# Kernel optimization log

Measured on AMD Instinct MI355X. Metric: run time of the kernel, lower is better.

The kernel has to match this reference:

```python
import jax, jax.numpy as jnp
import numpy as np

B = 512
INPUT_DIM = 1536
MAMBA_DIM = 1024
OUTPUT_DIM = 1024
D_STATE = 128
D_CONV = 4
EXPAND = 2
HEADDIM = 64
D_INNER = EXPAND * MAMBA_DIM          # 2048, == d_ssm
NHEADS = D_INNER // HEADDIM           # 32
CONV_DIM = D_INNER + 2 * D_STATE      # 2304
D_IN_PROJ = 2 * D_INNER + 2 * D_STATE + NHEADS  # 4384 (d_mlp = 0)
EPS = 1e-5


def rms_norm(x, g):
    return x * jax.lax.rsqrt(jnp.mean(x * x, axis=-1, keepdims=True) + EPS) * g


def setup_inputs() -> dict:
    key = jax.random.key(0)
    ks = jax.random.split(key, 16)
    def lin(k, fan_in, shape):
        return jax.random.normal(k, shape, jnp.float32) / np.sqrt(fan_in)
    return {
        "x": jax.random.normal(ks[0], (B, INPUT_DIM), jnp.float32),
        "conv_state": jax.random.normal(ks[1], (B, CONV_DIM, D_CONV), jnp.float32),
        "ssm_state": jax.random.normal(ks[2], (B, NHEADS, HEADDIM, D_STATE), jnp.float32),
        # NormedLinear in_proj (Linear + RMSNorm + SiLU)
        "w_in": lin(ks[3], INPUT_DIM, (INPUT_DIM, MAMBA_DIM)),
        "b_in": jnp.zeros((MAMBA_DIM,), jnp.float32),
        "g_in": jnp.ones((MAMBA_DIM,), jnp.float32),
        # Mamba2 params
        "W_inproj": lin(ks[4], MAMBA_DIM, (MAMBA_DIM, D_IN_PROJ)),
        "conv_w": lin(ks[5], D_CONV, (CONV_DIM, D_CONV)),
        "conv_b": jnp.zeros((CONV_DIM,), jnp.float32),
        "A_log": jnp.log(jax.random.uniform(ks[6], (NHEADS,), jnp.float32, 1.0, 16.0)),
        "dt_bias": 0.1 * jax.random.normal(ks[7], (NHEADS,), jnp.float32),
        "D": jnp.ones((NHEADS,), jnp.float32),
        "W_mamba_out": lin(ks[8], D_INNER, (D_INNER, MAMBA_DIM)),
        # outer out_proj Linear + RMSNorm
        "w_out": lin(ks[9], MAMBA_DIM, (MAMBA_DIM, OUTPUT_DIM)),
        "b_out": jnp.zeros((OUTPUT_DIM,), jnp.float32),
        "g_outnorm": jnp.ones((OUTPUT_DIM,), jnp.float32),
    }


def reference(x, conv_state, ssm_state, w_in, b_in, g_in, W_inproj, conv_w, conv_b,
              A_log, dt_bias, D, W_mamba_out, w_out, b_out, g_outnorm):
    # in_proj: Linear -> RMSNorm -> SiLU
    h = jax.nn.silu(rms_norm(x @ w_in + b_in, g_in))          # [B, MAMBA_DIM]
    zxbcdt = h @ W_inproj                                      # [B, D_IN_PROJ]
    z = zxbcdt[:, :D_INNER]                                    # [B, D_INNER]
    xbc = zxbcdt[:, D_INNER:D_INNER + CONV_DIM]                # [B, CONV_DIM]
    dt = zxbcdt[:, D_INNER + CONV_DIM:]                        # [B, NHEADS]
    # conv shift-and-sum
    conv_state_new = jnp.concatenate([conv_state[:, :, 1:], xbc[:, :, None]], axis=-1)
    xbc = jnp.sum(conv_state_new * conv_w[None], axis=-1) + conv_b
    xbc = jax.nn.silu(xbc)
    xh = xbc[:, :D_INNER].reshape(B, NHEADS, HEADDIM)          # [B, H, P]
    b = xbc[:, D_INNER:D_INNER + D_STATE]                      # [B, N]
    c = xbc[:, D_INNER + D_STATE:]                             # [B, N]
    # SSM step
    a = -jnp.exp(A_log)                                        # [H]
    dt = jax.nn.softplus(dt + dt_bias)                         # [B, H]
    da = jnp.exp(dt * a)                                       # [B, H]
    dbx = jnp.einsum('bh,bn,bhp->bhpn', dt, b, xh)
    ssm_state_new = ssm_state * da[:, :, None, None] + dbx     # [B, H, P, N]
    y = jnp.einsum('bhpn,bn->bhp', ssm_state_new, c)
    y = y + D[None, :, None] * xh
    y = y.reshape(B, D_INNER) * jax.nn.silu(z)
    y = y @ W_mamba_out                                        # [B, MAMBA_DIM]
    # outer projection + norm
    y = rms_norm(y @ w_out + b_out, g_outnorm)                 # [B, OUTPUT_DIM]
    return y, conv_state_new, ssm_state_new
```

## Files before the change

### kernel.cpp

```cpp
#include <hip/hip_runtime.h>
#include <hip/hip_bf16.h>

#define B_SZ      512
#define INPUT_DIM 1536
#define MAMBA_DIM 1024
#define OUT_DIM   1024
#define D_STATE   128
#define HEADDIM   64
#define D_INNER   2048
#define NHEADS    32
#define CONV_DIM  2304
#define D_IN_PROJ 4384

__device__ __forceinline__ float silu_precise(float x) {
    return x / (1.0f + expf(-x));
}

__global__ __launch_bounds__(256) void sgemm_kernel(
    const float* __restrict__ A, const float* __restrict__ W,
    const float* __restrict__ bias, float* __restrict__ C,
    int M, int N, int K)
{
    __shared__ float As[32][64];
    __shared__ float Bs[32][64];

    const int t   = threadIdx.x;
    const int bn0 = blockIdx.x * 64;
    const int bm0 = blockIdx.y * 64;
    const int tr  = t >> 4;
    const int tc  = t & 15;

    float acc[4][4] = {};

    for (int k0 = 0; k0 < K; k0 += 32) {
        #pragma unroll
        for (int i = 0; i < 2; ++i) {
            int idx = t + i * 256;
            int row = idx >> 3;
            int c4  = (idx & 7) * 4;
            float4 v = *(const float4*)(A + (size_t)(bm0 + row) * K + k0 + c4);
            As[c4 + 0][row] = v.x;
            As[c4 + 1][row] = v.y;
            As[c4 + 2][row] = v.z;
            As[c4 + 3][row] = v.w;
        }
        #pragma unroll
        for (int i = 0; i < 2; ++i) {
            int idx = t + i * 256;
            int kr  = idx >> 4;
            int c4  = (idx & 15) * 4;
            int n   = bn0 + c4;
            float4 v = make_float4(0.f, 0.f, 0.f, 0.f);
            if (n < N) v = *(const float4*)(W + (size_t)(k0 + kr) * N + n);
            *(float4*)&Bs[kr][c4] = v;
        }
        __syncthreads();

        #pragma unroll
        for (int k = 0; k < 32; ++k) {
            float4 a = *(const float4*)&As[k][tr * 4];
            float4 b = *(const float4*)&Bs[k][tc * 4];
            float av[4] = {a.x, a.y, a.z, a.w};
            float bv[4] = {b.x, b.y, b.z, b.w};
            #pragma unroll
            for (int i = 0; i < 4; ++i)
                #pragma unroll
                for (int j = 0; j < 4; ++j)
                    acc[i][j] += av[i] * bv[j];
        }
        __syncthreads();
    }

    #pragma unroll
    for (int i = 0; i < 4; ++i) {
        int m = bm0 + tr * 4 + i;
        #pragma unroll
        for (int j = 0; j < 4; ++j) {
            int n = bn0 + tc * 4 + j;
            if (n < N) {
                float v = acc[i][j];
                if (bias) v += bias[n];
                C[(size_t)m * N + n] = v;
            }
        }
    }
}

template <bool SILU>
__global__ __launch_bounds__(256) void rmsnorm_kernel(
    const float* __restrict__ X, const float* __restrict__ g,
    float* __restrict__ Y)
{
    const int row = blockIdx.x;
    const float* x = X + (size_t)row * 1024;
    float4 v = *(const float4*)(x + threadIdx.x * 4);
    float ss = v.x * v.x + v.y * v.y + v.z * v.z + v.w * v.w;
    #pragma unroll
    for (int off = 32; off > 0; off >>= 1) ss += __shfl_down(ss, off);

    __shared__ float wsum[4];
    const int wid = threadIdx.x >> 6;
    if ((threadIdx.x & 63) == 0) wsum[wid] = ss;
    __syncthreads();
    const float tot = wsum[0] + wsum[1] + wsum[2] + wsum[3];
    const float rs = 1.0f / sqrtf(tot * (1.0f / 1024.0f) + 1e-5f);

    float4 gv = *(const float4*)(g + threadIdx.x * 4);
    float4 o;
    o.x = v.x * rs * gv.x;
    o.y = v.y * rs * gv.y;
    o.z = v.z * rs * gv.z;
    o.w = v.w * rs * gv.w;
    if (SILU) {
        o.x = silu_precise(o.x);
        o.y = silu_precise(o.y);
        o.z = silu_precise(o.z);
        o.w = silu_precise(o.w);
    }
    *(float4*)(Y + (size_t)row * 1024 + threadIdx.x * 4) = o;
}

__global__ __launch_bounds__(256) void conv_kernel(
    const float* __restrict__ conv_state, const float* __restrict__ zx,
    const float* __restrict__ conv_w, const float* __restrict__ conv_b,
    float* __restrict__ conv_state_out, float* __restrict__ xbc_out)
{
    const int gid = blockIdx.x * 256 + threadIdx.x;
    const int b = gid / CONV_DIM;
    const int c = gid - b * CONV_DIM;

    float4 cs = *(const float4*)(conv_state + (size_t)gid * 4);
    float xn = zx[(size_t)b * D_IN_PROJ + D_INNER + c];
    float4 w = *(const float4*)(conv_w + c * 4);

    float s = cs.y * w.x + cs.z * w.y + cs.w * w.z + xn * w.w + conv_b[c];
    float r = silu_precise(s);

    float4 o = make_float4(cs.y, cs.z, cs.w, xn);
    *(float4*)(conv_state_out + (size_t)gid * 4) = o;
    xbc_out[gid] = r;
}

__global__ __launch_bounds__(256) void ssm_kernel(
    const float* __restrict__ ssm_state, const float* __restrict__ xbc,
    const float* __restrict__ zx, const float* __restrict__ A_log,
    const float* __restrict__ dt_bias, const float* __restrict__ Dp,
    float* __restrict__ ssm_out, float* __restrict__ yz)
{
    const int h = blockIdx.x;
    const int b = blockIdx.y;
    const int t = threadIdx.x;
    const int lane_n = t & 31;
    const int n0 = lane_n * 4;
    const int pg = t >> 5;

    float dtv = zx[(size_t)b * D_IN_PROJ + (D_INNER + CONV_DIM) + h] + dt_bias[h];
    dtv = (dtv > 20.f) ? dtv : log1pf(expf(dtv));
    const float a  = -expf(A_log[h]);
    const float da = expf(dtv * a);
    const float dcoef = Dp[h];

    const float* xrow = xbc + (size_t)b * CONV_DIM;

    const float4 bb = *(const float4*)(xrow + D_INNER + n0);
    const float4 cc = *(const float4*)(xrow + D_INNER + D_STATE + n0);

    const size_t slab = ((size_t)b * NHEADS + h) * (HEADDIM * D_STATE);
    const float* sp = ssm_state + slab;
    float*       so = ssm_out   + slab;

    #pragma unroll
    for (int i = 0; i < 8; ++i) {
        const int p = pg + i * 8;
        const float xh = xrow[h * HEADDIM + p];
        const float coef = dtv * xh;

        const size_t off = (size_t)p * D_STATE + n0;
        float4 s = *(const float4*)(sp + off);
        float4 ns;
        ns.x = s.x * da + coef * bb.x;
        ns.y = s.y * da + coef * bb.y;
        ns.z = s.z * da + coef * bb.z;
        ns.w = s.w * da + coef * bb.w;
        *(float4*)(so + off) = ns;

        float y = ns.x * cc.x + ns.y * cc.y + ns.z * cc.z + ns.w * cc.w;
        y += __shfl_xor(y, 16);
        y += __shfl_xor(y, 8);
        y += __shfl_xor(y, 4);
        y += __shfl_xor(y, 2);
        y += __shfl_xor(y, 1);

        if (lane_n == 0) {
            float z = zx[(size_t)b * D_IN_PROJ + h * HEADDIM + p];
            float yv = y + dcoef * xh;
            yz[(size_t)b * D_INNER + h * HEADDIM + p] = yv * silu_precise(z);
        }
    }
}


extern "C" void kernel_launch(void* const* d_in, const int* in_sizes, int n_in,
                              void* d_out, int out_size, void* d_ws, size_t ws_size,
                              hipStream_t stream)
{
    const float* x          = (const float*)d_in[0];
    const float* conv_state = (const float*)d_in[1];
    const float* ssm_state  = (const float*)d_in[2];
    const float* w_in       = (const float*)d_in[3];
    const float* b_in       = (const float*)d_in[4];
    const float* g_in       = (const float*)d_in[5];
    const float* W_inproj   = (const float*)d_in[6];
    const float* conv_w     = (const float*)d_in[7];
    const float* conv_b     = (const float*)d_in[8];
    const float* A_log      = (const float*)d_in[9];
    const float* dt_bias    = (const float*)d_in[10];
    const float* Dp         = (const float*)d_in[11];
    const float* W_mamba_out= (const float*)d_in[12];
    const float* w_out      = (const float*)d_in[13];
    const float* b_out      = (const float*)d_in[14];
    const float* g_outnorm  = (const float*)d_in[15];

    float* out_y    = (float*)d_out;
    float* out_conv = out_y + (size_t)B_SZ * OUT_DIM;
    float* out_ssm  = out_conv + (size_t)B_SZ * CONV_DIM * 4;

    float* ws  = (float*)d_ws;
    float* t1  = ws;
    float* h   = t1  + (size_t)B_SZ * MAMBA_DIM;
    float* zx  = h   + (size_t)B_SZ * MAMBA_DIM;
    float* xbc = zx  + (size_t)B_SZ * D_IN_PROJ;
    float* yzb = xbc + (size_t)B_SZ * CONV_DIM;
    float* u   = yzb + (size_t)B_SZ * D_INNER;
    float* t2  = u   + (size_t)B_SZ * MAMBA_DIM;

    sgemm_kernel<<<dim3(MAMBA_DIM / 64, B_SZ / 64), 256, 0, stream>>>(
        x, w_in, b_in, t1, B_SZ, MAMBA_DIM, INPUT_DIM);
    rmsnorm_kernel<true><<<B_SZ, 256, 0, stream>>>(t1, g_in, h);
    sgemm_kernel<<<dim3((D_IN_PROJ + 63) / 64, B_SZ / 64), 256, 0, stream>>>(
        h, W_inproj, nullptr, zx, B_SZ, D_IN_PROJ, MAMBA_DIM);
    conv_kernel<<<(B_SZ * CONV_DIM) / 256, 256, 0, stream>>>(
        conv_state, zx, conv_w, conv_b, out_conv, xbc);
    ssm_kernel<<<dim3(NHEADS, B_SZ), 256, 0, stream>>>(
        ssm_state, xbc, zx, A_log, dt_bias, Dp, out_ssm, yzb);
    sgemm_kernel<<<dim3(MAMBA_DIM / 64, B_SZ / 64), 256, 0, stream>>>(
        yzb, W_mamba_out, nullptr, u, B_SZ, MAMBA_DIM, D_INNER);
    sgemm_kernel<<<dim3(OUT_DIM / 64, B_SZ / 64), 256, 0, stream>>>(
        u, w_out, b_out, t2, B_SZ, OUT_DIM, MAMBA_DIM);
    rmsnorm_kernel<false><<<B_SZ, 256, 0, stream>>>(t2, g_outnorm, out_y);
}
```

Baseline: 1.321 ms.

## Split-K all GEMMs with atomic accumulation into zeroed workspace

Every GEMM now splits the K dimension across a third grid axis (8 or 4 slices), and partial tiles are accumulated into the output with float atomicAdd. A zero kernel clears the contiguous GEMM output buffers first. The workspace is reordered so those buffers sit together, and the A shared tile is padded to cut bank conflicts. The aim is more blocks to fill the GPU's many compute units, since the original grids were only 128–552 blocks. In exchange it adds atomic traffic, an extra zeroing pass, and non-deterministic summation order.

New measurement: 1.273 ms. 1.04x faster.

```diff
diff --git a/kernel.cpp b/kernel.cpp
--- a/kernel.cpp
+++ b/kernel.cpp
@@ -16,23 +16,33 @@
     return x / (1.0f + expf(-x));
 }
 
-__global__ __launch_bounds__(256) void sgemm_kernel(
+__global__ __launch_bounds__(256) void zero_kernel(float4* __restrict__ p, int n4)
+{
+    int i = blockIdx.x * 256 + threadIdx.x;
+    const int stride = gridDim.x * 256;
+    const float4 z = make_float4(0.f, 0.f, 0.f, 0.f);
+    for (; i < n4; i += stride) p[i] = z;
+}
+
+__global__ __launch_bounds__(256) void sgemm_splitk_kernel(
     const float* __restrict__ A, const float* __restrict__ W,
     const float* __restrict__ bias, float* __restrict__ C,
-    int M, int N, int K)
-{
-    __shared__ float As[32][64];
+    int M, int N, int K, int Kper)
+{
+    __shared__ float As[32][68];
     __shared__ float Bs[32][64];
 
     const int t   = threadIdx.x;
     const int bn0 = blockIdx.x * 64;
     const int bm0 = blockIdx.y * 64;
+    const int kz0 = blockIdx.z * Kper;
     const int tr  = t >> 4;
     const int tc  = t & 15;
 
     float acc[4][4] = {};
 
-    for (int k0 = 0; k0 < K; k0 += 32) {
+    for (int kk = 0; kk < Kper; kk += 32) {
+        const int k0 = kz0 + kk;
         #pragma unroll
         for (int i = 0; i < 2; ++i) {
             int idx = t + i * 256;
@@ -71,6 +81,7 @@
         __syncthreads();
     }
 
+    const bool addb = (bias != nullptr) && (blockIdx.z == 0);
     #pragma unroll
     for (int i = 0; i < 4; ++i) {
         int m = bm0 + tr * 4 + i;
@@ -79,8 +90,8 @@
             int n = bn0 + tc * 4 + j;
             if (n < N) {
                 float v = acc[i][j];
-                if (bias) v += bias[n];
-                C[(size_t)m * N + n] = v;
+                if (addb) v += bias[n];
+                atomicAdd(&C[(size_t)m * N + n], v);
             }
         }
     }
@@ -227,25 +238,29 @@
 
     float* ws  = (float*)d_ws;
     float* t1  = ws;
-    float* h   = t1  + (size_t)B_SZ * MAMBA_DIM;
-    float* zx  = h   + (size_t)B_SZ * MAMBA_DIM;
-    float* xbc = zx  + (size_t)B_SZ * D_IN_PROJ;
+    float* zx  = t1  + (size_t)B_SZ * MAMBA_DIM;
+    float* u   = zx  + (size_t)B_SZ * D_IN_PROJ;
+    float* t2  = u   + (size_t)B_SZ * MAMBA_DIM;
+    float* h   = t2  + (size_t)B_SZ * MAMBA_DIM;
+    float* xbc = h   + (size_t)B_SZ * MAMBA_DIM;
     float* yzb = xbc + (size_t)B_SZ * CONV_DIM;
-    float* u   = yzb + (size_t)B_SZ * D_INNER;
-    float* t2  = u   + (size_t)B_SZ * MAMBA_DIM;
-
-    sgemm_kernel<<<dim3(MAMBA_DIM / 64, B_SZ / 64), 256, 0, stream>>>(
-        x, w_in, b_in, t1, B_SZ, MAMBA_DIM, INPUT_DIM);
+
+    const int gemm_out_floats = B_SZ * (MAMBA_DIM + D_IN_PROJ + MAMBA_DIM + MAMBA_DIM);
+
+    zero_kernel<<<2048, 256, 0, stream>>>((float4*)ws, gemm_out_floats / 4);
+
+    sgemm_splitk_kernel<<<dim3(MAMBA_DIM / 64, B_SZ / 64, 8), 256, 0, stream>>>(
+        x, w_in, b_in, t1, B_SZ, MAMBA_DIM, INPUT_DIM, INPUT_DIM / 8);
     rmsnorm_kernel<true><<<B_SZ, 256, 0, stream>>>(t1, g_in, h);
-    sgemm_kernel<<<dim3((D_IN_PROJ + 63) / 64, B_SZ / 64), 256, 0, stream>>>(
-        h, W_inproj, nullptr, zx, B_SZ, D_IN_PROJ, MAMBA_DIM);
+    sgemm_splitk_kernel<<<dim3((D_IN_PROJ + 63) / 64, B_SZ / 64, 4), 256, 0, stream>>>(
+        h, W_inproj, nullptr, zx, B_SZ, D_IN_PROJ, MAMBA_DIM, MAMBA_DIM / 4);
     conv_kernel<<<(B_SZ * CONV_DIM) / 256, 256, 0, stream>>>(
         conv_state, zx, conv_w, conv_b, out_conv, xbc);
     ssm_kernel<<<dim3(NHEADS, B_SZ), 256, 0, stream>>>(
         ssm_state, xbc, zx, A_log, dt_bias, Dp, out_ssm, yzb);
-    sgemm_kernel<<<dim3(MAMBA_DIM / 64, B_SZ / 64), 256, 0, stream>>>(
-        yzb, W_mamba_out, nullptr, u, B_SZ, MAMBA_DIM, D_INNER);
-    sgemm_kernel<<<dim3(OUT_DIM / 64, B_SZ / 64), 256, 0, stream>>>(
-        u, w_out, b_out, t2, B_SZ, OUT_DIM, MAMBA_DIM);
+    sgemm_splitk_kernel<<<dim3(MAMBA_DIM / 64, B_SZ / 64, 8), 256, 0, stream>>>(
+        yzb, W_mamba_out, nullptr, u, B_SZ, MAMBA_DIM, D_INNER, D_INNER / 8);
+    sgemm_splitk_kernel<<<dim3(OUT_DIM / 64, B_SZ / 64, 8), 256, 0, stream>>>(
+        u, w_out, b_out, t2, B_SZ, OUT_DIM, MAMBA_DIM, MAMBA_DIM / 8);
     rmsnorm_kernel<false><<<B_SZ, 256, 0, stream>>>(t2, g_outnorm, out_y);
 }
```
